# Kernel tuning notes

Measured on AMD Instinct MI355X. Metric: run time of the kernel, lower is better.

## Reference

```python
import jax, jax.numpy as jnp
import numpy as np
import math

N_HEADS = 8
TANH_CLIP = 10.0
TEMP = 1.0


def setup_inputs() -> dict:
    key = jax.random.key(0)
    ks = jax.random.split(key, 8)
    B, N, D = 256, 2048, 128
    node_embeddings = jax.random.normal(ks[0], (B, N, D), dtype=jnp.float32)
    W_node = jax.random.normal(ks[1], (D, 3 * D), dtype=jnp.float32) / math.sqrt(D)
    W_fixed = jax.random.normal(ks[2], (D, D), dtype=jnp.float32) / math.sqrt(D)
    W_step = jax.random.normal(ks[3], (2 * D, D), dtype=jnp.float32) / math.sqrt(2 * D)
    W_out = jax.random.normal(ks[4], (D, D), dtype=jnp.float32) / math.sqrt(D)
    first_idx = jax.random.randint(ks[5], (B,), 0, N, dtype=jnp.int32)
    last_idx = jax.random.randint(ks[6], (B,), 0, N, dtype=jnp.int32)
    mask = jax.random.bernoulli(ks[7], 0.5, (B, N))
    mask = mask.at[:, 0].set(False)  # guarantee at least one feasible node per row
    return {"node_embeddings": node_embeddings, "W_node": W_node, "W_fixed": W_fixed,
            "W_step": W_step, "W_out": W_out, "first_idx": first_idx,
            "last_idx": last_idx, "mask": mask}


def reference(node_embeddings, W_node, W_fixed, W_step, W_out, first_idx, last_idx, mask):
    B, N, D = node_embeddings.shape
    H = N_HEADS
    hd = D // H  # key_dim = val_dim = embed_dim / n_heads
    neg_inf = -jnp.inf

    # --- _precompute ---
    graph_embed = node_embeddings.mean(axis=1)                # [B, D]
    fixed_context = graph_embed @ W_fixed                     # [B, D]
    proj = node_embeddings @ W_node                           # [B, N, 3D]
    gK, gV, logit_K = jnp.split(proj, 3, axis=-1)             # each [B, N, D]
    gK = gK.reshape(B, N, H, hd).transpose(2, 0, 1, 3)        # [H, B, N, hd]
    gV = gV.reshape(B, N, H, hd).transpose(2, 0, 1, 3)        # [H, B, N, hd]

    # --- step context: cat(first node emb, last node emb) ---
    first_emb = jnp.take_along_axis(node_embeddings, first_idx[:, None, None].astype(jnp.int32), axis=1)[:, 0]  # [B, D]
    last_emb = jnp.take_along_axis(node_embeddings, last_idx[:, None, None].astype(jnp.int32), axis=1)[:, 0]
    step_ctx = jnp.concatenate([first_emb, last_emb], axis=-1)  # [B, 2D]
    query = fixed_context + step_ctx @ W_step                 # [B, D]

    # --- glimpse multi-head attention (n_query = 1, masked inner) ---
    Q = query.reshape(B, H, hd).transpose(1, 0, 2)            # [H, B, hd]
    compat = jnp.einsum('hbd,hbnd->hbn', Q, gK) / math.sqrt(hd)  # [H, B, N]
    compat = jnp.where(mask[None, :, :], neg_inf, compat)     # mask_inner=True
    attn = jax.nn.softmax(compat, axis=-1)
    heads = jnp.einsum('hbn,hbnd->hbd', attn, gV)             # [H, B, hd]
    glimpse = heads.transpose(1, 0, 2).reshape(B, D) @ W_out  # project_out, [B, D]

    # --- logits with tanh clipping and masking ---
    logits = jnp.einsum('bd,bnd->bn', glimpse, logit_K) / math.sqrt(D)  # [B, N]
    logits = jnp.tanh(logits) * TANH_CLIP
    logits = jnp.where(mask, neg_inf, logits)                 # mask_logits=True
    log_p = jax.nn.log_softmax(logits / TEMP, axis=-1)        # [B, N]
    return log_p
```

## Files before the change

kernel.cpp:

```cpp
#include <hip/hip_runtime.h>
#include <math.h>

#define B_ 256
#define N_ 2048
#define D_ 128

#define NEG_HUGE (-1.0e30f)

#define WSA_STRIDE 1040
#define WSA_SIZE (B_ * 8 * WSA_STRIDE)
#define WSB_OFF WSA_SIZE
#define WSB_SIZE (B_ * 8 * 2)
#define WSC_OFF (WSB_OFF + WSB_SIZE)

typedef __attribute__((ext_vector_type(8))) short bf16x8;
typedef __attribute__((ext_vector_type(4))) float f32x4;
typedef __attribute__((ext_vector_type(4))) unsigned short u16x4;
typedef __attribute__((ext_vector_type(2))) int i32x2;

__device__ __forceinline__ float wave_max64(float v) {
#pragma unroll
  for (int off = 32; off > 0; off >>= 1) v = fmaxf(v, __shfl_xor(v, off, 64));
  return v;
}
__device__ __forceinline__ float wave_sum64(float v) {
#pragma unroll
  for (int off = 32; off > 0; off >>= 1) v += __shfl_xor(v, off, 64);
  return v;
}
__device__ __forceinline__ unsigned short bf16rne(float f) {
  unsigned u = __float_as_uint(f);
  u += 0x7FFFu + ((u >> 16) & 1u);
  return (unsigned short)(u >> 16);
}

__global__ void __launch_bounds__(256) k_prep(const float* __restrict__ emb,
                                              float* __restrict__ buf) {
  const int b = blockIdx.x, s = blockIdx.y, t = threadIdx.x;
  const int f4 = t & 31, g = t >> 5;
  const size_t rowbase = (size_t)b * N_;
  float4 acc = make_float4(0.f, 0.f, 0.f, 0.f);
  int n = s * 256 + g;
#pragma unroll 8
  for (int i = 0; i < 32; ++i, n += 8) {
    const float4 v = *(const float4*)(emb + (rowbase + n) * D_ + f4 * 4);
    acc.x += v.x; acc.y += v.y; acc.z += v.z; acc.w += v.w;
  }
  __shared__ float4 red[256];
  red[t] = acc;
  __syncthreads();
  if (g == 0) {
    float4 r = red[f4];
#pragma unroll
    for (int j = 1; j < 8; ++j) {
      const float4 a = red[j * 32 + f4];
      r.x += a.x; r.y += a.y; r.z += a.z; r.w += a.w;
    }
    *(float4*)(buf + (size_t)b * N_ + s * 128 + f4 * 4) = r;
  }
}

__global__ void __launch_bounds__(384) k_query(const float* __restrict__ emb,
                                               const float* __restrict__ Wfix,
                                               const float* __restrict__ Wstep,
                                               const float* __restrict__ Wnode,
                                               const int* __restrict__ fidx,
                                               const int* __restrict__ lidx,
                                               float* __restrict__ buf) {
  const int b = blockIdx.x, t = threadIdx.x;
  __shared__ float x[384];
  __shared__ float part[3][128];
  __shared__ float q[128];

  if (t < 128) {
    float ssum = 0.f;
#pragma unroll
    for (int i = 0; i < 8; ++i) ssum += buf[(size_t)b * N_ + i * 128 + t];
    x[t] = ssum * (1.0f / 2048.0f);
  } else if (t < 256) {
    x[t] = emb[((size_t)b * N_ + fidx[b]) * D_ + (t - 128)];
  } else {
    x[t] = emb[((size_t)b * N_ + lidx[b]) * D_ + (t - 256)];
  }
  __syncthreads();

  {
    const int seg = t >> 7, j = t & 127;
    const float* xs = &x[seg * 128];
    const float* Wp = (seg == 0) ? (Wfix + j) : (Wstep + (seg == 1 ? 0 : 128 * 128) + j);
    float acc = 0.f;
#pragma unroll 8
    for (int k = 0; k < 128; ++k) acc = fmaf(xs[k], Wp[(size_t)k * 128], acc);
    part[seg][j] = acc;
  }
  __syncthreads();
  if (t < 128) q[t] = part[0][t] + part[1][t] + part[2][t];
  __syncthreads();

  if (t < 128) {
    const float* wrow = Wnode + (size_t)t * 384;
#pragma unroll
    for (int h = 0; h < 8; ++h) {
      float a = 0.f;
#pragma unroll
      for (int k = 0; k < 16; ++k) a = fmaf(q[h * 16 + k], wrow[h * 16 + k], a);
      buf[(size_t)b * N_ + 1024 + h * 128 + t] = a * 0.25f;
    }
  }
}

__global__ void __launch_bounds__(256) k_attn_m(const float* __restrict__ emb,
                                                const unsigned char* __restrict__ mask,
                                                const float* __restrict__ buf,
                                                float* __restrict__ wsA) {
  const int b = B_ - 1 - (int)blockIdx.x, s = 7 - (int)blockIdx.y;
  const int t = threadIdx.x;
  const int lane = t & 63, w = t >> 6;
  const int lg = lane >> 4, lc = lane & 15;

  __shared__ __align__(16) unsigned short eR[9216];
  __shared__ __align__(16) unsigned short pT[16 * 72];
  __shared__ float red0[4][16];
  __shared__ float red1[4][16];
  __shared__ float resc_s[16];
  __shared__ unsigned char mask_s[64];

  bf16x8 bq[4];
#pragma unroll
  for (int ks = 0; ks < 4; ++ks)
#pragma unroll
    for (int j = 0; j < 8; ++j) bq[ks][j] = 0;
  if (lc < 8) {
    const float* qrow = buf + (size_t)b * N_ + 1024 + lc * 128;
#pragma unroll
    for (int ks = 0; ks < 4; ++ks)
#pragma unroll
      for (int j = 0; j < 8; ++j)
        bq[ks][j] = (short)bf16rne(qrow[32 * ks + 8 * lg + j]);
  }

  float m_run = -INFINITY, l_run = 0.f;
  f32x4 wacc0 = {0.f, 0.f, 0.f, 0.f}, wacc1 = {0.f, 0.f, 0.f, 0.f};
  const float* embb = emb + ((size_t)b * N_ + s * 256) * D_;
  const unsigned char* mrow = mask + (size_t)b * N_ + s * 256;

  for (int tile = 0; tile < 4; ++tile) {
    {
      const float* src = embb + (size_t)tile * 64 * D_;
#pragma unroll
      for (int i = 0; i < 4; ++i) {
        const int gid = t + 256 * i;
        const int n = gid >> 4, d0 = (gid & 15) * 8;
        const float4 v0 = *(const float4*)(src + (size_t)n * D_ + d0);
        const float4 v1 = *(const float4*)(src + (size_t)n * D_ + d0 + 4);
        bf16x8 ev;
        ev[0] = (short)bf16rne(v0.x); ev[1] = (short)bf16rne(v0.y);
        ev[2] = (short)bf16rne(v0.z); ev[3] = (short)bf16rne(v0.w);
        ev[4] = (short)bf16rne(v1.x); ev[5] = (short)bf16rne(v1.y);
        ev[6] = (short)bf16rne(v1.z); ev[7] = (short)bf16rne(v1.w);
        const int widx = ((n >> 2) * 8 + (d0 >> 4)) * 72 + ((n & 3) << 4) + (d0 & 15);
        *(bf16x8*)&eR[widx] = ev;
      }
      if (t < 64) mask_s[t] = mrow[tile * 64 + t];
    }
    __syncthreads();

    f32x4 sAcc = {0.f, 0.f, 0.f, 0.f};
#pragma unroll
    for (int ks = 0; ks < 4; ++ks) {
      const int aidx = ((4 * w + (lc >> 2)) * 8 + 2 * ks + (lg >> 1)) * 72 +
                       ((lc & 3) << 4) + ((lg & 1) << 3);
      const bf16x8 af = *(const bf16x8*)&eR[aidx];
      sAcc = __builtin_amdgcn_mfma_f32_16x16x32_bf16(af, bq[ks], sAcc, 0, 0, 0);
    }

    float sv[4];
    bool mk[4];
    float tmax = -INFINITY;
#pragma unroll
    for (int r = 0; r < 4; ++r) {
      mk[r] = mask_s[16 * w + 4 * lg + r] != 0;
      sv[r] = mk[r] ? -INFINITY : sAcc[r];
      tmax = fmaxf(tmax, sv[r]);
    }
    tmax = fmaxf(tmax, __shfl_xor(tmax, 16, 64));
    tmax = fmaxf(tmax, __shfl_xor(tmax, 32, 64));
    if (lane < 16) red0[w][lc] = tmax;
    __syncthreads();

    const float m_tile = fmaxf(fmaxf(red0[0][lc], red0[1][lc]),
                               fmaxf(red0[2][lc], red0[3][lc]));
    const float m_new = fmaxf(m_run, m_tile);
    const float rsc = (m_new == -INFINITY) ? 1.f : __expf(m_run - m_new);
    float psum = 0.f;
    unsigned short pu[4];
#pragma unroll
    for (int r = 0; r < 4; ++r) {
      const float p = mk[r] ? 0.f : __expf(sv[r] - m_new);
      psum += p;
      pu[r] = bf16rne(p);
    }
    m_run = m_new;
    psum += __shfl_xor(psum, 16, 64);
    psum += __shfl_xor(psum, 32, 64);
    if (lane < 16) red1[w][lc] = psum;
    *(u16x4*)&pT[lc * 72 + 16 * w + 4 * lg] = (u16x4){pu[0], pu[1], pu[2], pu[3]};
    if (t < 16) resc_s[t] = rsc;
    __syncthreads();

    l_run = l_run * rsc + (red1[0][lc] + red1[1][lc] + red1[2][lc] + red1[3][lc]);

    {
      const float r0f = resc_s[4 * lg + 0], r1f = resc_s[4 * lg + 1];
      const float r2f = resc_s[4 * lg + 2], r3f = resc_s[4 * lg + 3];
      wacc0[0] *= r0f; wacc0[1] *= r1f; wacc0[2] *= r2f; wacc0[3] *= r3f;
      wacc1[0] *= r0f; wacc1[1] *= r1f; wacc1[2] *= r2f; wacc1[3] *= r3f;
    }

    i32x2 tb0a, tb0b, tb1a, tb1b, tb2a, tb2b, tb3a, tb3b;
    {
      const unsigned base00 = (unsigned)(unsigned long long)
          &eR[((0 + 2 * lg) * 8 + w) * 72 + lc];
      const unsigned base01 = (unsigned)(unsigned long long)
          &eR[((0 + 2 * lg) * 8 + (w + 4)) * 72 + lc];
      const unsigned base10 = (unsigned)(unsigned long long)
          &eR[((8 + 2 * lg) * 8 + w) * 72 + lc];
      const unsigned base11 = (unsigned)(unsigned long long)
          &eR[((8 + 2 * lg) * 8 + (w + 4)) * 72 + lc];
      asm volatile("ds_read_b64_tr_b16 %0, %2 offset:0\n\t"
                   "ds_read_b64_tr_b16 %1, %2 offset:1152"
                   : "=v"(tb0a), "=v"(tb0b) : "v"(base00));
      asm volatile("ds_read_b64_tr_b16 %0, %2 offset:0\n\t"
                   "ds_read_b64_tr_b16 %1, %2 offset:1152"
                   : "=v"(tb1a), "=v"(tb1b) : "v"(base01));
      asm volatile("ds_read_b64_tr_b16 %0, %2 offset:0\n\t"
                   "ds_read_b64_tr_b16 %1, %2 offset:1152"
                   : "=v"(tb2a), "=v"(tb2b) : "v"(base10));
      asm volatile("ds_read_b64_tr_b16 %0, %2 offset:0\n\t"
                   "ds_read_b64_tr_b16 %1, %2 offset:1152"
                   : "=v"(tb3a), "=v"(tb3b) : "v"(base11));
      asm volatile("s_waitcnt lgkmcnt(0)" ::: "memory");
      __builtin_amdgcn_sched_barrier(0);
    }
    {
      const bf16x8 pa0 = *(const bf16x8*)&pT[lc * 72 + 8 * lg];
      const bf16x8 pa1 = *(const bf16x8*)&pT[lc * 72 + 32 + 8 * lg];
      union { i32x2 d[2]; bf16x8 v; } u;
      u.d[0] = tb0a; u.d[1] = tb0b;
      wacc0 = __builtin_amdgcn_mfma_f32_16x16x32_bf16(pa0, u.v, wacc0, 0, 0, 0);
      u.d[0] = tb1a; u.d[1] = tb1b;
      wacc1 = __builtin_amdgcn_mfma_f32_16x16x32_bf16(pa0, u.v, wacc1, 0, 0, 0);
      u.d[0] = tb2a; u.d[1] = tb2b;
      wacc0 = __builtin_amdgcn_mfma_f32_16x16x32_bf16(pa1, u.v, wacc0, 0, 0, 0);
      u.d[0] = tb3a; u.d[1] = tb3b;
      wacc1 = __builtin_amdgcn_mfma_f32_16x16x32_bf16(pa1, u.v, wacc1, 0, 0, 0);
    }
    __syncthreads();
  }

  float* dst = wsA + (size_t)(b * 8 + s) * WSA_STRIDE;
  if (lg < 2) {
#pragma unroll
    for (int r = 0; r < 4; ++r) {
      const int h = 4 * lg + r;
      dst[16 + h * 128 + 16 * w + lc] = wacc0[r];
      dst[16 + h * 128 + 16 * (w + 4) + lc] = wacc1[r];
    }
  }
  if (t < 8) { dst[t] = m_run; dst[8 + t] = l_run; }
}

__global__ void __launch_bounds__(256) k_attn_comb(const float* __restrict__ Wnode,
                                                   const float* __restrict__ Wout,
                                                   const float* __restrict__ wsA,
                                                   float* __restrict__ wsC) {
  const int b = blockIdx.x, t = threadIdx.x;
  const int j = t & 127, hh = t >> 7;
  const float* base = wsA + (size_t)b * 8 * WSA_STRIDE;
  __shared__ float Ls[8], scale[8][8];
  __shared__ float wl[8 * 128], heads[128], glim[128];
  __shared__ float part2[2][128];

  if (t < 8) {
    float M = -INFINITY;
#pragma unroll
    for (int s = 0; s < 8; ++s) M = fmaxf(M, base[s * WSA_STRIDE + t]);
    float L = 0.f;
#pragma unroll
    for (int s = 0; s < 8; ++s) {
      const float m = base[s * WSA_STRIDE + t];
      const float sc = (m == -INFINITY) ? 0.f : __expf(m - M);
      scale[s][t] = sc;
      L = fmaf(base[s * WSA_STRIDE + 8 + t], sc, L);
    }
    Ls[t] = L;
  }
  __syncthreads();

#pragma unroll
  for (int k = 0; k < 4; ++k) {
    const int idx = t + 256 * k;
    const int h = idx >> 7, d = idx & 127;
    float acc = 0.f;
#pragma unroll
    for (int s = 0; s < 8; ++s)
      acc = fmaf(scale[s][h], base[s * WSA_STRIDE + 16 + h * 128 + d], acc);
    wl[idx] = acc;
  }
  __syncthreads();

  {
    const int h = j >> 4, kk = j & 15;
    const float* wp = Wnode + 128 + h * 16 + kk;
    float acc = 0.f;
#pragma unroll 8
    for (int d = 64 * hh; d < 64 * hh + 64; ++d)
      acc = fmaf(wl[h * 128 + d], wp[(size_t)d * 384], acc);
    part2[hh][j] = acc;
  }
  __syncthreads();
  if (t < 128) heads[t] = (part2[0][t] + part2[1][t]) / Ls[t >> 4];
  __syncthreads();

  {
    float acc = 0.f;
#pragma unroll 8
    for (int k = 64 * hh; k < 64 * hh + 64; ++k)
      acc = fmaf(heads[k], Wout[(size_t)k * 128 + j], acc);
    part2[hh][j] = acc;
  }
  __syncthreads();
  if (t < 128) glim[t] = part2[0][t] + part2[1][t];
  __syncthreads();

  {
    const float* wr = Wnode + (size_t)j * 384 + 256;
    float acc = 0.f;
#pragma unroll 8
    for (int k = 64 * hh; k < 64 * hh + 64; ++k)
      acc = fmaf(wr[k], glim[k], acc);
    part2[hh][j] = acc;
  }
  __syncthreads();
  if (t < 128)
    wsC[(size_t)b * 128 + t] = (part2[0][t] + part2[1][t]) * 0.08838834764831845f;
}

__global__ void __launch_bounds__(256) k_logits_part(const float* __restrict__ emb,
                                                     const unsigned char* __restrict__ mask,
                                                     const float* __restrict__ wsC,
                                                     float* __restrict__ buf,
                                                     float* __restrict__ wsB) {
  const int b = blockIdx.x, s = blockIdx.y;
  const int t = threadIdx.x, lane = t & 63, w = t >> 6;
  __shared__ float lg[64];
  const float4 cf = ((const float4*)(wsC + (size_t)b * 128))[t & 31];
  const float* embb = emb + ((size_t)b * N_ + s * 256) * D_;
  const unsigned char* mrow = mask + (size_t)b * N_ + s * 256;
  float mr = NEG_HUGE, sr = 0.f;

  for (int tile = 0; tile < 4; ++tile) {
    const int n0 = tile * 64;
#pragma unroll
    for (int i = 0; i < 8; ++i) {
      const int gid = t + 256 * i;
      const int r = gid >> 5, c = (gid & 31) * 4;
      const float4 e = *(const float4*)(embb + (size_t)(n0 + r) * D_ + c);
      float p = fmaf(e.x, cf.x, fmaf(e.y, cf.y, fmaf(e.z, cf.z, e.w * cf.w)));
      p += __shfl_xor(p, 16, 64);
      p += __shfl_xor(p, 8, 64);
      p += __shfl_xor(p, 4, 64);
      p += __shfl_xor(p, 2, 64);
      p += __shfl_xor(p, 1, 64);
      if ((t & 31) == 0) lg[r] = p;
    }
    __syncthreads();

    const bool mk = mrow[n0 + lane] != 0;
    const float x = lg[lane];
    const float ex = __expf(2.f * x);
    const float val = mk ? NEG_HUGE : (10.f - __fdividef(20.f, ex + 1.f));
    const float tm = wave_max64(val);
    const float mn = fmaxf(mr, tm);
    sr = sr * __expf(mr - mn) + wave_sum64(mk ? 0.f : __expf(val - mn));
    mr = mn;
    if (w == 0) buf[(size_t)b * N_ + s * 256 + n0 + lane] = val;
    __syncthreads();
  }
  if (t == 0) {
    wsB[(size_t)(b * 8 + s) * 2] = mr;
    wsB[(size_t)(b * 8 + s) * 2 + 1] = sr;
  }
}

__global__ void __launch_bounds__(256) k_norm(const float* __restrict__ wsB,
                                              float* __restrict__ buf) {
  const int b = blockIdx.x, s = blockIdx.y, t = threadIdx.x;
  float M = NEG_HUGE;
#pragma unroll
  for (int q = 0; q < 8; ++q) M = fmaxf(M, wsB[(size_t)(b * 8 + q) * 2]);
  float S = 0.f;
#pragma unroll
  for (int q = 0; q < 8; ++q) {
    const float m = wsB[(size_t)(b * 8 + q) * 2];
    S += wsB[(size_t)(b * 8 + q) * 2 + 1] * __expf(m - M);
  }
  const float LS = M + logf(S);
  const size_t idx = (size_t)b * N_ + s * 256 + t;
  const float v = buf[idx];
  buf[idx] = (v <= -1.0e29f) ? NEG_HUGE : (v - LS);
}

extern "C" void kernel_launch(void* const* d_in, const int* in_sizes, int n_in,
                              void* d_out, int out_size, void* d_ws, size_t ws_size,
                              hipStream_t stream) {
  (void)in_sizes; (void)n_in; (void)out_size; (void)ws_size;
  const float* emb = (const float*)d_in[0];
  const float* Wnode = (const float*)d_in[1];
  const float* Wfix = (const float*)d_in[2];
  const float* Wstep = (const float*)d_in[3];
  const float* Wout = (const float*)d_in[4];
  const int* fidx = (const int*)d_in[5];
  const int* lidx = (const int*)d_in[6];
  const unsigned char* mask = (const unsigned char*)d_in[7];
  float* buf = (float*)d_out;
  float* ws = (float*)d_ws;

  k_prep<<<dim3(B_, 8), 256, 0, stream>>>(emb, buf);
  k_query<<<B_, 384, 0, stream>>>(emb, Wfix, Wstep, Wnode, fidx, lidx, buf);
  k_attn_m<<<dim3(B_, 8), 256, 0, stream>>>(emb, mask, buf, ws);
  k_attn_comb<<<B_, 256, 0, stream>>>(Wnode, Wout, ws, ws + WSC_OFF);
  k_logits_part<<<dim3(B_, 8), 256, 0, stream>>>(emb, mask, ws + WSC_OFF, buf, ws + WSB_OFF);
  k_norm<<<dim3(B_, 8), 256, 0, stream>>>(ws + WSB_OFF, buf);
}
```

Baseline: 161.1 us.

## Fuse all stages into persistent kernel with grid barriers and bf16 embedding copy

Replaces the six-kernel pipeline with one persistent kernel of 1024 blocks that runs the stages in sequence, separated by software grid barriers built on atomics. The first pass, which reads the fp32 embeddings to compute the mean, also writes a bf16 copy to workspace. The attention and logits passes then read that copy instead of re-reading the fp32 data, roughly halving their memory traffic. In exchange it adds a 128 MB workspace write, a deadlock risk if the 1024 blocks are not all resident at once, and reduced precision in the logits dot product.

```diff
diff --git a/kernel.cpp b/kernel.cpp
--- a/kernel.cpp
+++ b/kernel.cpp
@@ -4,14 +4,22 @@
 #define B_ 256
 #define N_ 2048
 #define D_ 128
+#define NSEG 2048
+#define GRID_MEGA 1024
 
 #define NEG_HUGE (-1.0e30f)
 
+#define WSE_BYTES ((size_t)B_ * N_ * D_ * 2)
+#define WSQ_OFF 262144
+#define WSA_OFF 524288
+#define WSB_OFF_M 2654208
+#define WSC_OFF_M 2658304
+#define BAR_OFF 2691072
+#define WS_NEED_BYTES (WSE_BYTES + (size_t)(BAR_OFF + 8) * 4)
+
 #define WSA_STRIDE 1040
-#define WSA_SIZE (B_ * 8 * WSA_STRIDE)
-#define WSB_OFF WSA_SIZE
-#define WSB_SIZE (B_ * 8 * 2)
-#define WSC_OFF (WSB_OFF + WSB_SIZE)
+#define FB_WSB_OFF (B_ * 8 * WSA_STRIDE)
+#define FB_WSC_OFF (FB_WSB_OFF + B_ * 8 * 2)
 
 typedef __attribute__((ext_vector_type(8))) short bf16x8;
 typedef __attribute__((ext_vector_type(4))) float f32x4;
@@ -32,6 +40,409 @@
   unsigned u = __float_as_uint(f);
   u += 0x7FFFu + ((u >> 16) & 1u);
   return (unsigned short)(u >> 16);
+}
+__device__ __forceinline__ float bflo(unsigned u) { return __uint_as_float(u << 16); }
+__device__ __forceinline__ float bfhi(unsigned u) { return __uint_as_float(u & 0xFFFF0000u); }
+
+__device__ __forceinline__ void grid_barrier(unsigned* bar, unsigned nb) {
+  __syncthreads();
+  if (threadIdx.x == 0) {
+    const unsigned mygen = atomicAdd(&bar[1], 0u);
+    __threadfence();
+    const unsigned arrived = atomicAdd(&bar[0], 1u) + 1u;
+    if (arrived == nb) {
+      atomicExch(&bar[0], 0u);
+      __threadfence();
+      atomicAdd(&bar[1], 1u);
+    } else {
+      while (atomicAdd(&bar[1], 0u) == mygen) { __builtin_amdgcn_s_sleep(8); }
+    }
+    __threadfence();
+  }
+  __syncthreads();
+}
+
+__global__ void __launch_bounds__(256, 4) k_mega(
+    const float* __restrict__ emb, const float* __restrict__ Wnode,
+    const float* __restrict__ Wfix, const float* __restrict__ Wstep,
+    const float* __restrict__ Wout, const int* __restrict__ fidx,
+    const int* __restrict__ lidx, const unsigned char* __restrict__ mask,
+    float* __restrict__ buf, unsigned short* __restrict__ wsE,
+    float* __restrict__ wsF, unsigned* __restrict__ bar) {
+  const int g = blockIdx.x, t = threadIdx.x;
+  const unsigned nb = gridDim.x;
+  float* wsM = wsF;
+  float* wsQ = wsF + WSQ_OFF;
+  float* wsA = wsF + WSA_OFF;
+  float* wsB = wsF + WSB_OFF_M;
+  float* wsC = wsF + WSC_OFF_M;
+
+  __shared__ __align__(16) unsigned char smem[21504];
+
+  for (int seg = g; seg < NSEG; seg += nb) {
+    const int b = seg >> 3, s = seg & 7;
+    const int f4 = t & 31, gg = t >> 5;
+    const size_t rowbase = (size_t)b * N_;
+    float4 acc = make_float4(0.f, 0.f, 0.f, 0.f);
+    int n = s * 256 + gg;
+#pragma unroll 8
+    for (int i = 0; i < 32; ++i, n += 8) {
+      const float4 v = *(const float4*)(emb + (rowbase + n) * D_ + f4 * 4);
+      acc.x += v.x; acc.y += v.y; acc.z += v.z; acc.w += v.w;
+      ushort4 o;
+      o.x = bf16rne(v.x); o.y = bf16rne(v.y); o.z = bf16rne(v.z); o.w = bf16rne(v.w);
+      *(ushort4*)(wsE + (rowbase + n) * D_ + f4 * 4) = o;
+    }
+    float4* red = (float4*)smem;
+    __syncthreads();
+    red[t] = acc;
+    __syncthreads();
+    if (gg == 0) {
+      float4 r = red[f4];
+#pragma unroll
+      for (int j = 1; j < 8; ++j) {
+        const float4 a = red[j * 32 + f4];
+        r.x += a.x; r.y += a.y; r.z += a.z; r.w += a.w;
+      }
+      *(float4*)(wsM + (size_t)(b * 8 + s) * 128 + f4 * 4) = r;
+    }
+  }
+  grid_barrier(bar, nb);
+
+  for (int b = g; b < B_; b += nb) {
+    float* ge = (float*)smem;
+    float* fe = ge + 128;
+    float* le = ge + 256;
+    float* pq = ge + 384;
+    float* q = ge + 640;
+    if (t < 128) {
+      float ssum = 0.f;
+#pragma unroll
+      for (int i = 0; i < 8; ++i) ssum += wsM[(size_t)(b * 8 + i) * 128 + t];
+      ge[t] = ssum * (1.0f / 2048.0f);
+      fe[t] = emb[((size_t)b * N_ + fidx[b]) * D_ + t];
+      le[t] = emb[((size_t)b * N_ + lidx[b]) * D_ + t];
+    }
+    __syncthreads();
+    {
+      const int j = t & 127, h2 = t >> 7;
+      float acc = 0.f;
+#pragma unroll 4
+      for (int k = 64 * h2; k < 64 * h2 + 64; ++k) {
+        acc = fmaf(ge[k], Wfix[k * 128 + j], acc);
+        acc = fmaf(fe[k], Wstep[k * 128 + j], acc);
+        acc = fmaf(le[k], Wstep[(128 + k) * 128 + j], acc);
+      }
+      pq[h2 * 128 + j] = acc;
+    }
+    __syncthreads();
+    if (t < 128) q[t] = pq[t] + pq[128 + t];
+    __syncthreads();
+    if (t < 128) {
+      const float* wrow = Wnode + (size_t)t * 384;
+#pragma unroll
+      for (int h = 0; h < 8; ++h) {
+        float a = 0.f;
+#pragma unroll
+        for (int k = 0; k < 16; ++k) a = fmaf(q[h * 16 + k], wrow[h * 16 + k], a);
+        wsQ[(size_t)b * 1024 + h * 128 + t] = a * 0.25f;
+      }
+    }
+    __syncthreads();
+  }
+  grid_barrier(bar, nb);
+
+  {
+    unsigned short* eR = (unsigned short*)smem;
+    unsigned short* pT = (unsigned short*)(smem + 18432);
+    float* red0 = (float*)(smem + 20736);
+    float* red1 = (float*)(smem + 20992);
+    float* resc = (float*)(smem + 21248);
+    unsigned char* mask_s = smem + 21312;
+    const int lane = t & 63, w = t >> 6;
+    const int lg = lane >> 4, lc = lane & 15;
+
+    for (int seg = g; seg < NSEG; seg += nb) {
+      const int b = seg >> 3, s = seg & 7;
+      bf16x8 bq[4];
+#pragma unroll
+      for (int ks = 0; ks < 4; ++ks)
+#pragma unroll
+        for (int j = 0; j < 8; ++j) bq[ks][j] = 0;
+      if (lc < 8) {
+        const float* qrow = wsQ + (size_t)b * 1024 + lc * 128;
+#pragma unroll
+        for (int ks = 0; ks < 4; ++ks)
+#pragma unroll
+          for (int j = 0; j < 8; ++j)
+            bq[ks][j] = (short)bf16rne(qrow[32 * ks + 8 * lg + j]);
+      }
+
+      float m_run = -INFINITY, l_run = 0.f;
+      f32x4 wacc0 = {0.f, 0.f, 0.f, 0.f}, wacc1 = {0.f, 0.f, 0.f, 0.f};
+      const unsigned short* embB = wsE + ((size_t)b * N_ + s * 256) * D_;
+      const unsigned char* mrow = mask + (size_t)b * N_ + s * 256;
+
+      for (int tile = 0; tile < 4; ++tile) {
+        __syncthreads();
+#pragma unroll
+        for (int i = 0; i < 4; ++i) {
+          const int gid = t + 256 * i;
+          const int n = gid >> 4, d0 = (gid & 15) * 8;
+          const int widx =
+              ((n >> 2) * 8 + (d0 >> 4)) * 72 + ((n & 3) << 4) + (d0 & 15);
+          const uint4 u =
+              *(const uint4*)(embB + ((size_t)tile * 64 + n) * D_ + d0);
+          *(uint4*)&eR[widx] = u;
+        }
+        if (t < 64) mask_s[t] = mrow[tile * 64 + t];
+        __syncthreads();
+
+        f32x4 sAcc = {0.f, 0.f, 0.f, 0.f};
+#pragma unroll
+        for (int ks = 0; ks < 4; ++ks) {
+          const int aidx = ((4 * w + (lc >> 2)) * 8 + 2 * ks + (lg >> 1)) * 72 +
+                           ((lc & 3) << 4) + ((lg & 1) << 3);
+          const bf16x8 af = *(const bf16x8*)&eR[aidx];
+          sAcc = __builtin_amdgcn_mfma_f32_16x16x32_bf16(af, bq[ks], sAcc, 0, 0, 0);
+        }
+
+        float sv[4];
+        bool mk[4];
+        float tmax = -INFINITY;
+#pragma unroll
+        for (int r = 0; r < 4; ++r) {
+          mk[r] = mask_s[16 * w + 4 * lg + r] != 0;
+          sv[r] = mk[r] ? -INFINITY : sAcc[r];
+          tmax = fmaxf(tmax, sv[r]);
+        }
+        tmax = fmaxf(tmax, __shfl_xor(tmax, 16, 64));
+        tmax = fmaxf(tmax, __shfl_xor(tmax, 32, 64));
+        if (lane < 16) red0[w * 16 + lc] = tmax;
+        __syncthreads();
+
+        const float m_tile = fmaxf(fmaxf(red0[lc], red0[16 + lc]),
+                                   fmaxf(red0[32 + lc], red0[48 + lc]));
+        const float m_new = fmaxf(m_run, m_tile);
+        const float rsc = (m_new == -INFINITY) ? 1.f : __expf(m_run - m_new);
+        float psum = 0.f;
+        unsigned short pu[4];
+#pragma unroll
+        for (int r = 0; r < 4; ++r) {
+          const float p = mk[r] ? 0.f : __expf(sv[r] - m_new);
+          psum += p;
+          pu[r] = bf16rne(p);
+        }
+        m_run = m_new;
+        psum += __shfl_xor(psum, 16, 64);
+        psum += __shfl_xor(psum, 32, 64);
+        if (lane < 16) red1[w * 16 + lc] = psum;
+        *(u16x4*)&pT[lc * 72 + 16 * w + 4 * lg] = (u16x4){pu[0], pu[1], pu[2], pu[3]};
+        if (t < 16) resc[t] = rsc;
+        __syncthreads();
+
+        l_run = l_run * rsc +
+                (red1[lc] + red1[16 + lc] + red1[32 + lc] + red1[48 + lc]);
+        {
+          const float r0f = resc[4 * lg + 0], r1f = resc[4 * lg + 1];
+          const float r2f = resc[4 * lg + 2], r3f = resc[4 * lg + 3];
+          wacc0[0] *= r0f; wacc0[1] *= r1f; wacc0[2] *= r2f; wacc0[3] *= r3f;
+          wacc1[0] *= r0f; wacc1[1] *= r1f; wacc1[2] *= r2f; wacc1[3] *= r3f;
+        }
+
+        i32x2 tb0a, tb0b, tb1a, tb1b, tb2a, tb2b, tb3a, tb3b;
+        {
+          const unsigned base00 = (unsigned)(unsigned long long)
+              &eR[((0 + 2 * lg) * 8 + w) * 72 + lc];
+          const unsigned base01 = (unsigned)(unsigned long long)
+              &eR[((0 + 2 * lg) * 8 + (w + 4)) * 72 + lc];
+          const unsigned base10 = (unsigned)(unsigned long long)
+              &eR[((8 + 2 * lg) * 8 + w) * 72 + lc];
+          const unsigned base11 = (unsigned)(unsigned long long)
+              &eR[((8 + 2 * lg) * 8 + (w + 4)) * 72 + lc];
+          asm volatile("ds_read_b64_tr_b16 %0, %2 offset:0\n\t"
+                       "ds_read_b64_tr_b16 %1, %2 offset:1152"
+                       : "=v"(tb0a), "=v"(tb0b) : "v"(base00));
+          asm volatile("ds_read_b64_tr_b16 %0, %2 offset:0\n\t"
+                       "ds_read_b64_tr_b16 %1, %2 offset:1152"
+                       : "=v"(tb1a), "=v"(tb1b) : "v"(base01));
+          asm volatile("ds_read_b64_tr_b16 %0, %2 offset:0\n\t"
+                       "ds_read_b64_tr_b16 %1, %2 offset:1152"
+                       : "=v"(tb2a), "=v"(tb2b) : "v"(base10));
+          asm volatile("ds_read_b64_tr_b16 %0, %2 offset:0\n\t"
+                       "ds_read_b64_tr_b16 %1, %2 offset:1152"
+                       : "=v"(tb3a), "=v"(tb3b) : "v"(base11));
+          asm volatile("s_waitcnt lgkmcnt(0)" ::: "memory");
+          __builtin_amdgcn_sched_barrier(0);
+        }
+        {
+          const bf16x8 pa0 = *(const bf16x8*)&pT[lc * 72 + 8 * lg];
+          const bf16x8 pa1 = *(const bf16x8*)&pT[lc * 72 + 32 + 8 * lg];
+          union { i32x2 d[2]; bf16x8 v; } u;
+          u.d[0] = tb0a; u.d[1] = tb0b;
+          wacc0 = __builtin_amdgcn_mfma_f32_16x16x32_bf16(pa0, u.v, wacc0, 0, 0, 0);
+          u.d[0] = tb1a; u.d[1] = tb1b;
+          wacc1 = __builtin_amdgcn_mfma_f32_16x16x32_bf16(pa0, u.v, wacc1, 0, 0, 0);
+          u.d[0] = tb2a; u.d[1] = tb2b;
+          wacc0 = __builtin_amdgcn_mfma_f32_16x16x32_bf16(pa1, u.v, wacc0, 0, 0, 0);
+          u.d[0] = tb3a; u.d[1] = tb3b;
+          wacc1 = __builtin_amdgcn_mfma_f32_16x16x32_bf16(pa1, u.v, wacc1, 0, 0, 0);
+        }
+        __syncthreads();
+      }
+
+      float* dst = wsA + (size_t)(b * 8 + s) * WSA_STRIDE;
+      if (lg < 2) {
+#pragma unroll
+        for (int r = 0; r < 4; ++r) {
+          const int h = 4 * lg + r;
+          dst[16 + h * 128 + 16 * w + lc] = wacc0[r];
+          dst[16 + h * 128 + 16 * (w + 4) + lc] = wacc1[r];
+        }
+      }
+      if (t < 8) { dst[t] = m_run; dst[8 + t] = l_run; }
+      __syncthreads();
+    }
+  }
+  grid_barrier(bar, nb);
+
+  for (int b = g; b < B_; b += nb) {
+    float* Ls = (float*)smem;
+    float* scale = Ls + 8;
+    float* wl = scale + 64;
+    float* heads = wl + 1024;
+    float* glim = heads + 128;
+    float* p2 = glim + 128;
+    const int j = t & 127, hh = t >> 7;
+    const float* base = wsA + (size_t)b * 8 * WSA_STRIDE;
+
+    if (t < 8) {
+      float M = -INFINITY;
+#pragma unroll
+      for (int s = 0; s < 8; ++s) M = fmaxf(M, base[s * WSA_STRIDE + t]);
+      float L = 0.f;
+#pragma unroll
+      for (int s = 0; s < 8; ++s) {
+        const float m = base[s * WSA_STRIDE + t];
+        const float sc = (m == -INFINITY) ? 0.f : __expf(m - M);
+        scale[s * 8 + t] = sc;
+        L = fmaf(base[s * WSA_STRIDE + 8 + t], sc, L);
+      }
+      Ls[t] = L;
+    }
+    __syncthreads();
+#pragma unroll
+    for (int k = 0; k < 4; ++k) {
+      const int idx = t + 256 * k;
+      const int h = idx >> 7, d = idx & 127;
+      float acc = 0.f;
+#pragma unroll
+      for (int s = 0; s < 8; ++s)
+        acc = fmaf(scale[s * 8 + h], base[s * WSA_STRIDE + 16 + h * 128 + d], acc);
+      wl[idx] = acc;
+    }
+    __syncthreads();
+    {
+      const int h = j >> 4, kk = j & 15;
+      const float* wp = Wnode + 128 + h * 16 + kk;
+      float acc = 0.f;
+#pragma unroll 8
+      for (int d = 64 * hh; d < 64 * hh + 64; ++d)
+        acc = fmaf(wl[h * 128 + d], wp[(size_t)d * 384], acc);
+      p2[hh * 128 + j] = acc;
+    }
+    __syncthreads();
+    if (t < 128) heads[t] = (p2[t] + p2[128 + t]) / Ls[t >> 4];
+    __syncthreads();
+    {
+      float acc = 0.f;
+#pragma unroll 8
+      for (int k = 64 * hh; k < 64 * hh + 64; ++k)
+        acc = fmaf(heads[k], Wout[(size_t)k * 128 + j], acc);
+      p2[hh * 128 + j] = acc;
+    }
+    __syncthreads();
+    if (t < 128) glim[t] = p2[t] + p2[128 + t];
+    __syncthreads();
+    {
+      const float* wr = Wnode + (size_t)j * 384 + 256;
+      float acc = 0.f;
+#pragma unroll 8
+      for (int k = 64 * hh; k < 64 * hh + 64; ++k) acc = fmaf(wr[k], glim[k], acc);
+      p2[hh * 128 + j] = acc;
+    }
+    __syncthreads();
+    if (t < 128)
+      wsC[(size_t)b * 128 + t] = (p2[t] + p2[128 + t]) * 0.08838834764831845f;
+    __syncthreads();
+  }
+  grid_barrier(bar, nb);
+
+  {
+    float* lgs = (float*)smem;
+    const int lane = t & 63, w4 = t >> 6;
+    for (int seg = g; seg < NSEG; seg += nb) {
+      const int b = seg >> 3, s = seg & 7;
+      const float4* c4 = (const float4*)(wsC + (size_t)b * 128);
+      const float4 cfa = c4[(t & 15) * 2];
+      const float4 cfb = c4[(t & 15) * 2 + 1];
+      const unsigned short* embB = wsE + ((size_t)b * N_ + s * 256) * D_;
+      const unsigned char* mrow = mask + (size_t)b * N_ + s * 256;
+      float mr = NEG_HUGE, sr = 0.f;
+      for (int tile = 0; tile < 4; ++tile) {
+        const int n0 = tile * 64;
+#pragma unroll
+        for (int i = 0; i < 4; ++i) {
+          const int gid = t + 256 * i;
+          const int r = gid >> 4, c8 = (gid & 15) * 8;
+          const uint4 u = *(const uint4*)(embB + (size_t)(n0 + r) * D_ + c8);
+          float p = bflo(u.x) * cfa.x + bfhi(u.x) * cfa.y;
+          p = fmaf(bflo(u.y), cfa.z, p); p = fmaf(bfhi(u.y), cfa.w, p);
+          p = fmaf(bflo(u.z), cfb.x, p); p = fmaf(bfhi(u.z), cfb.y, p);
+          p = fmaf(bflo(u.w), cfb.z, p); p = fmaf(bfhi(u.w), cfb.w, p);
+          p += __shfl_xor(p, 8, 64);
+          p += __shfl_xor(p, 4, 64);
+          p += __shfl_xor(p, 2, 64);
+          p += __shfl_xor(p, 1, 64);
+          if ((t & 15) == 0) lgs[r] = p;
+        }
+        __syncthreads();
+        const bool mk = mrow[n0 + lane] != 0;
+        const float x = lgs[lane];
+        const float ex = __expf(2.f * x);
+        const float val = mk ? NEG_HUGE : (10.f - __fdividef(20.f, ex + 1.f));
+        const float tm = wave_max64(val);
+        const float mn = fmaxf(mr, tm);
+        sr = sr * __expf(mr - mn) + wave_sum64(mk ? 0.f : __expf(val - mn));
+        mr = mn;
+        if (w4 == 0) buf[(size_t)b * N_ + s * 256 + n0 + lane] = val;
+        __syncthreads();
+      }
+      if (t == 0) {
+        wsB[(size_t)(b * 8 + s) * 2] = mr;
+        wsB[(size_t)(b * 8 + s) * 2 + 1] = sr;
+      }
+      __syncthreads();
+    }
+  }
+  grid_barrier(bar, nb);
+
+  for (int seg = g; seg < NSEG; seg += nb) {
+    const int b = seg >> 3, s = seg & 7;
+    float M = NEG_HUGE;
+#pragma unroll
+    for (int qq = 0; qq < 8; ++qq) M = fmaxf(M, wsB[(size_t)(b * 8 + qq) * 2]);
+    float S = 0.f;
+#pragma unroll
+    for (int qq = 0; qq < 8; ++qq) {
+      const float m = wsB[(size_t)(b * 8 + qq) * 2];
+      S += wsB[(size_t)(b * 8 + qq) * 2 + 1] * __expf(m - M);
+    }
+    const float LS = M + logf(S);
+    const size_t idx = (size_t)b * N_ + s * 256 + t;
+    const float v = buf[idx];
+    buf[idx] = (v <= -1.0e29f) ? NEG_HUGE : (v - LS);
+  }
 }
 
 __global__ void __launch_bounds__(256) k_prep(const float* __restrict__ emb,
@@ -71,7 +482,6 @@
   __shared__ float x[384];
   __shared__ float part[3][128];
   __shared__ float q[128];
-
   if (t < 128) {
     float ssum = 0.f;
 #pragma unroll
@@ -83,7 +493,6 @@
     x[t] = emb[((size_t)b * N_ + lidx[b]) * D_ + (t - 256)];
   }
   __syncthreads();
-
   {
     const int seg = t >> 7, j = t & 127;
     const float* xs = &x[seg * 128];
@@ -96,7 +505,6 @@
   __syncthreads();
   if (t < 128) q[t] = part[0][t] + part[1][t] + part[2][t];
   __syncthreads();
-
   if (t < 128) {
     const float* wrow = Wnode + (size_t)t * 384;
 #pragma unroll
@@ -113,18 +521,16 @@
                                                 const unsigned char* __restrict__ mask,
                                                 const float* __restrict__ buf,
                                                 float* __restrict__ wsA) {
-  const int b = B_ - 1 - (int)blockIdx.x, s = 7 - (int)blockIdx.y;
+  const int b = blockIdx.x, s = blockIdx.y;
   const int t = threadIdx.x;
   const int lane = t & 63, w = t >> 6;
   const int lg = lane >> 4, lc = lane & 15;
-
   __shared__ __align__(16) unsigned short eR[9216];
   __shared__ __align__(16) unsigned short pT[16 * 72];
   __shared__ float red0[4][16];
   __shared__ float red1[4][16];
   __shared__ float resc_s[16];
   __shared__ unsigned char mask_s[64];
-
   bf16x8 bq[4];
 #pragma unroll
   for (int ks = 0; ks < 4; ++ks)
@@ -138,12 +544,10 @@
       for (int j = 0; j < 8; ++j)
         bq[ks][j] = (short)bf16rne(qrow[32 * ks + 8 * lg + j]);
   }
-
   float m_run = -INFINITY, l_run = 0.f;
   f32x4 wacc0 = {0.f, 0.f, 0.f, 0.f}, wacc1 = {0.f, 0.f, 0.f, 0.f};
   const float* embb = emb + ((size_t)b * N_ + s * 256) * D_;
   const unsigned char* mrow = mask + (size_t)b * N_ + s * 256;
-
   for (int tile = 0; tile < 4; ++tile) {
     {
       const float* src = embb + (size_t)tile * 64 * D_;
@@ -164,7 +568,6 @@
       if (t < 64) mask_s[t] = mrow[tile * 64 + t];
     }
     __syncthreads();
-
     f32x4 sAcc = {0.f, 0.f, 0.f, 0.f};
 #pragma unroll
     for (int ks = 0; ks < 4; ++ks) {
@@ -173,7 +576,6 @@
       const bf16x8 af = *(const bf16x8*)&eR[aidx];
       sAcc = __builtin_amdgcn_mfma_f32_16x16x32_bf16(af, bq[ks], sAcc, 0, 0, 0);
     }
-
     float sv[4];
     bool mk[4];
     float tmax = -INFINITY;
@@ -187,7 +589,6 @@
     tmax = fmaxf(tmax, __shfl_xor(tmax, 32, 64));
     if (lane < 16) red0[w][lc] = tmax;
     __syncthreads();
-
     const float m_tile = fmaxf(fmaxf(red0[0][lc], red0[1][lc]),
                                fmaxf(red0[2][lc], red0[3][lc]));
     const float m_new = fmaxf(m_run, m_tile);
@@ -207,16 +608,13 @@
     *(u16x4*)&pT[lc * 72 + 16 * w + 4 * lg] = (u16x4){pu[0], pu[1], pu[2], pu[3]};
     if (t < 16) resc_s[t] = rsc;
     __syncthreads();
-
     l_run = l_run * rsc + (red1[0][lc] + red1[1][lc] + red1[2][lc] + red1[3][lc]);
-
     {
       const float r0f = resc_s[4 * lg + 0], r1f = resc_s[4 * lg + 1];
       const float r2f = resc_s[4 * lg + 2], r3f = resc_s[4 * lg + 3];
       wacc0[0] *= r0f; wacc0[1] *= r1f; wacc0[2] *= r2f; wacc0[3] *= r3f;
       wacc1[0] *= r0f; wacc1[1] *= r1f; wacc1[2] *= r2f; wacc1[3] *= r3f;
     }
-
     i32x2 tb0a, tb0b, tb1a, tb1b, tb2a, tb2b, tb3a, tb3b;
     {
       const unsigned base00 = (unsigned)(unsigned long long)
@@ -257,7 +655,6 @@
     }
     __syncthreads();
   }
-
   float* dst = wsA + (size_t)(b * 8 + s) * WSA_STRIDE;
   if (lg < 2) {
 #pragma unroll
@@ -280,7 +677,6 @@
   __shared__ float Ls[8], scale[8][8];
   __shared__ float wl[8 * 128], heads[128], glim[128];
   __shared__ float part2[2][128];
-
   if (t < 8) {
     float M = -INFINITY;
 #pragma unroll
@@ -296,7 +692,6 @@
     Ls[t] = L;
   }
   __syncthreads();
-
 #pragma unroll
   for (int k = 0; k < 4; ++k) {
     const int idx = t + 256 * k;
@@ -308,7 +703,6 @@
     wl[idx] = acc;
   }
   __syncthreads();
-
   {
     const int h = j >> 4, kk = j & 15;
     const float* wp = Wnode + 128 + h * 16 + kk;
@@ -321,7 +715,6 @@
   __syncthreads();
   if (t < 128) heads[t] = (part2[0][t] + part2[1][t]) / Ls[t >> 4];
   __syncthreads();
-
   {
     float acc = 0.f;
 #pragma unroll 8
@@ -332,13 +725,11 @@
   __syncthreads();
   if (t < 128) glim[t] = part2[0][t] + part2[1][t];
   __syncthreads();
-
   {
     const float* wr = Wnode + (size_t)j * 384 + 256;
     float acc = 0.f;
 #pragma unroll 8
-    for (int k = 64 * hh; k < 64 * hh + 64; ++k)
-      acc = fmaf(wr[k], glim[k], acc);
+    for (int k = 64 * hh; k < 64 * hh + 64; ++k) acc = fmaf(wr[k], glim[k], acc);
     part2[hh][j] = acc;
   }
   __syncthreads();
@@ -358,7 +749,6 @@
   const float* embb = emb + ((size_t)b * N_ + s * 256) * D_;
   const unsigned char* mrow = mask + (size_t)b * N_ + s * 256;
   float mr = NEG_HUGE, sr = 0.f;
-
   for (int tile = 0; tile < 4; ++tile) {
     const int n0 = tile * 64;
 #pragma unroll
@@ -375,7 +765,6 @@
       if ((t & 31) == 0) lg[r] = p;
     }
     __syncthreads();
-
     const bool mk = mrow[n0 + lane] != 0;
     const float x = lg[lane];
     const float ex = __expf(2.f * x);
@@ -414,7 +803,7 @@
 extern "C" void kernel_launch(void* const* d_in, const int* in_sizes, int n_in,
                               void* d_out, int out_size, void* d_ws, size_t ws_size,
                               hipStream_t stream) {
-  (void)in_sizes; (void)n_in; (void)out_size; (void)ws_size;
+  (void)in_sizes; (void)n_in; (void)out_size;
   const float* emb = (const float*)d_in[0];
   const float* Wnode = (const float*)d_in[1];
   const float* Wfix = (const float*)d_in[2];
@@ -424,12 +813,25 @@
   const int* lidx = (const int*)d_in[6];
   const unsigned char* mask = (const unsigned char*)d_in[7];
   float* buf = (float*)d_out;
-  float* ws = (float*)d_ws;
-
-  k_prep<<<dim3(B_, 8), 256, 0, stream>>>(emb, buf);
-  k_query<<<B_, 384, 0, stream>>>(emb, Wfix, Wstep, Wnode, fidx, lidx, buf);
-  k_attn_m<<<dim3(B_, 8), 256, 0, stream>>>(emb, mask, buf, ws);
-  k_attn_comb<<<B_, 256, 0, stream>>>(Wnode, Wout, ws, ws + WSC_OFF);
-  k_logits_part<<<dim3(B_, 8), 256, 0, stream>>>(emb, mask, ws + WSC_OFF, buf, ws + WSB_OFF);
-  k_norm<<<dim3(B_, 8), 256, 0, stream>>>(ws + WSB_OFF, buf);
-}
+
+  int occ = 0;
+  (void)hipOccupancyMaxActiveBlocksPerMultiprocessor(&occ, k_mega, 256, 0);
+
+  if (occ >= 4 && ws_size >= WS_NEED_BYTES) {
+    unsigned short* wsE = (unsigned short*)d_ws;
+    float* wsF = (float*)((char*)d_ws + WSE_BYTES);
+    unsigned* bar = (unsigned*)(wsF + BAR_OFF);
+    hipMemsetAsync(bar, 0, 8, stream);
+    k_mega<<<GRID_MEGA, 256, 0, stream>>>(emb, Wnode, Wfix, Wstep, Wout, fidx,
+                                          lidx, mask, buf, wsE, wsF, bar);
+  } else {
+    float* ws = (float*)d_ws;
+    k_prep<<<dim3(B_, 8), 256, 0, stream>>>(emb, buf);
+    k_query<<<B_, 384, 0, stream>>>(emb, Wfix, Wstep, Wnode, fidx, lidx, buf);
+    k_attn_m<<<dim3(B_, 8), 256, 0, stream>>>(emb, mask, buf, ws);
+    k_attn_comb<<<B_, 256, 0, stream>>>(Wnode, Wout, ws, ws + FB_WSC_OFF);
+    k_logits_part<<<dim3(B_, 8), 256, 0, stream>>>(emb, mask, ws + FB_WSC_OFF, buf,
+                                                   ws + FB_WSB_OFF);
+    k_norm<<<dim3(B_, 8), 256, 0, stream>>>(ws + FB_WSB_OFF, buf);
+  }
+}
```

Result: no change. 160.2 us (-0.6%).

## Fuse combine and normalize stages into last-arriving blocks via atomic counters

Applied to the files above, without the earlier changes.

Removes the separate k_attn_comb and k_norm launches. Each block increments a per-batch atomic counter, and the last of the 8 split blocks performs the cross-split combine (attention merge plus projections) or the final log-softmax normalization. This saves two kernel launches and their tail/ramp gaps. The cost is a memset for the counters and serialized tail work in one block per batch. The block index order reversal in k_attn_m is also dropped.

```diff
diff --git a/kernel.cpp b/kernel.cpp
--- a/kernel.cpp
+++ b/kernel.cpp
@@ -8,10 +8,10 @@
 #define NEG_HUGE (-1.0e30f)
 
 #define WSA_STRIDE 1040
-#define WSA_SIZE (B_ * 8 * WSA_STRIDE)
-#define WSB_OFF WSA_SIZE
-#define WSB_SIZE (B_ * 8 * 2)
-#define WSC_OFF (WSB_OFF + WSB_SIZE)
+#define WSB_OFF (B_ * 8 * WSA_STRIDE)
+#define WSC_OFF (WSB_OFF + B_ * 8 * 2)
+#define FLAGS_OFF (WSC_OFF + B_ * D_)
+#define WS_NEED_BYTES ((size_t)(FLAGS_OFF + 512) * 4)
 
 typedef __attribute__((ext_vector_type(8))) short bf16x8;
 typedef __attribute__((ext_vector_type(4))) float f32x4;
@@ -71,7 +71,6 @@
   __shared__ float x[384];
   __shared__ float part[3][128];
   __shared__ float q[128];
-
   if (t < 128) {
     float ssum = 0.f;
 #pragma unroll
@@ -83,7 +82,6 @@
     x[t] = emb[((size_t)b * N_ + lidx[b]) * D_ + (t - 256)];
   }
   __syncthreads();
-
   {
     const int seg = t >> 7, j = t & 127;
     const float* xs = &x[seg * 128];
@@ -96,7 +94,6 @@
   __syncthreads();
   if (t < 128) q[t] = part[0][t] + part[1][t] + part[2][t];
   __syncthreads();
-
   if (t < 128) {
     const float* wrow = Wnode + (size_t)t * 384;
 #pragma unroll
@@ -112,18 +109,22 @@
 __global__ void __launch_bounds__(256) k_attn_m(const float* __restrict__ emb,
                                                 const unsigned char* __restrict__ mask,
                                                 const float* __restrict__ buf,
-                                                float* __restrict__ wsA) {
-  const int b = B_ - 1 - (int)blockIdx.x, s = 7 - (int)blockIdx.y;
+                                                const float* __restrict__ Wnode,
+                                                const float* __restrict__ Wout,
+                                                float* __restrict__ wsA,
+                                                float* __restrict__ wsC,
+                                                unsigned* __restrict__ cprog) {
+  const int b = blockIdx.x, s = blockIdx.y;
   const int t = threadIdx.x;
   const int lane = t & 63, w = t >> 6;
   const int lg = lane >> 4, lc = lane & 15;
-
   __shared__ __align__(16) unsigned short eR[9216];
   __shared__ __align__(16) unsigned short pT[16 * 72];
-  __shared__ float red0[4][16];
-  __shared__ float red1[4][16];
-  __shared__ float resc_s[16];
+  __shared__ float red0[64];
+  __shared__ float red1[64];
+  __shared__ float resc[16];
   __shared__ unsigned char mask_s[64];
+  __shared__ unsigned sh_old;
 
   bf16x8 bq[4];
 #pragma unroll
@@ -138,12 +139,10 @@
       for (int j = 0; j < 8; ++j)
         bq[ks][j] = (short)bf16rne(qrow[32 * ks + 8 * lg + j]);
   }
-
   float m_run = -INFINITY, l_run = 0.f;
   f32x4 wacc0 = {0.f, 0.f, 0.f, 0.f}, wacc1 = {0.f, 0.f, 0.f, 0.f};
   const float* embb = emb + ((size_t)b * N_ + s * 256) * D_;
   const unsigned char* mrow = mask + (size_t)b * N_ + s * 256;
-
   for (int tile = 0; tile < 4; ++tile) {
     {
       const float* src = embb + (size_t)tile * 64 * D_;
@@ -164,7 +163,6 @@
       if (t < 64) mask_s[t] = mrow[tile * 64 + t];
     }
     __syncthreads();
-
     f32x4 sAcc = {0.f, 0.f, 0.f, 0.f};
 #pragma unroll
     for (int ks = 0; ks < 4; ++ks) {
@@ -173,7 +171,6 @@
       const bf16x8 af = *(const bf16x8*)&eR[aidx];
       sAcc = __builtin_amdgcn_mfma_f32_16x16x32_bf16(af, bq[ks], sAcc, 0, 0, 0);
     }
-
     float sv[4];
     bool mk[4];
     float tmax = -INFINITY;
@@ -185,11 +182,10 @@
     }
     tmax = fmaxf(tmax, __shfl_xor(tmax, 16, 64));
     tmax = fmaxf(tmax, __shfl_xor(tmax, 32, 64));
-    if (lane < 16) red0[w][lc] = tmax;
-    __syncthreads();
-
-    const float m_tile = fmaxf(fmaxf(red0[0][lc], red0[1][lc]),
-                               fmaxf(red0[2][lc], red0[3][lc]));
+    if (lane < 16) red0[w * 16 + lc] = tmax;
+    __syncthreads();
+    const float m_tile = fmaxf(fmaxf(red0[lc], red0[16 + lc]),
+                               fmaxf(red0[32 + lc], red0[48 + lc]));
     const float m_new = fmaxf(m_run, m_tile);
     const float rsc = (m_new == -INFINITY) ? 1.f : __expf(m_run - m_new);
     float psum = 0.f;
@@ -203,20 +199,17 @@
     m_run = m_new;
     psum += __shfl_xor(psum, 16, 64);
     psum += __shfl_xor(psum, 32, 64);
-    if (lane < 16) red1[w][lc] = psum;
+    if (lane < 16) red1[w * 16 + lc] = psum;
     *(u16x4*)&pT[lc * 72 + 16 * w + 4 * lg] = (u16x4){pu[0], pu[1], pu[2], pu[3]};
-    if (t < 16) resc_s[t] = rsc;
-    __syncthreads();
-
-    l_run = l_run * rsc + (red1[0][lc] + red1[1][lc] + red1[2][lc] + red1[3][lc]);
-
-    {
-      const float r0f = resc_s[4 * lg + 0], r1f = resc_s[4 * lg + 1];
-      const float r2f = resc_s[4 * lg + 2], r3f = resc_s[4 * lg + 3];
+    if (t < 16) resc[t] = rsc;
+    __syncthreads();
+    l_run = l_run * rsc + (red1[lc] + red1[16 + lc] + red1[32 + lc] + red1[48 + lc]);
+    {
+      const float r0f = resc[4 * lg + 0], r1f = resc[4 * lg + 1];
+      const float r2f = resc[4 * lg + 2], r3f = resc[4 * lg + 3];
       wacc0[0] *= r0f; wacc0[1] *= r1f; wacc0[2] *= r2f; wacc0[3] *= r3f;
       wacc1[0] *= r0f; wacc1[1] *= r1f; wacc1[2] *= r2f; wacc1[3] *= r3f;
     }
-
     i32x2 tb0a, tb0b, tb1a, tb1b, tb2a, tb2b, tb3a, tb3b;
     {
       const unsigned base00 = (unsigned)(unsigned long long)
@@ -257,7 +250,6 @@
     }
     __syncthreads();
   }
-
   float* dst = wsA + (size_t)(b * 8 + s) * WSA_STRIDE;
   if (lg < 2) {
 #pragma unroll
@@ -268,97 +260,95 @@
     }
   }
   if (t < 8) { dst[t] = m_run; dst[8 + t] = l_run; }
-}
-
-__global__ void __launch_bounds__(256) k_attn_comb(const float* __restrict__ Wnode,
-                                                   const float* __restrict__ Wout,
-                                                   const float* __restrict__ wsA,
-                                                   float* __restrict__ wsC) {
-  const int b = blockIdx.x, t = threadIdx.x;
-  const int j = t & 127, hh = t >> 7;
-  const float* base = wsA + (size_t)b * 8 * WSA_STRIDE;
-  __shared__ float Ls[8], scale[8][8];
-  __shared__ float wl[8 * 128], heads[128], glim[128];
-  __shared__ float part2[2][128];
-
-  if (t < 8) {
-    float M = -INFINITY;
-#pragma unroll
-    for (int s = 0; s < 8; ++s) M = fmaxf(M, base[s * WSA_STRIDE + t]);
-    float L = 0.f;
-#pragma unroll
-    for (int s = 0; s < 8; ++s) {
-      const float m = base[s * WSA_STRIDE + t];
-      const float sc = (m == -INFINITY) ? 0.f : __expf(m - M);
-      scale[s][t] = sc;
-      L = fmaf(base[s * WSA_STRIDE + 8 + t], sc, L);
-    }
-    Ls[t] = L;
-  }
-  __syncthreads();
-
-#pragma unroll
-  for (int k = 0; k < 4; ++k) {
-    const int idx = t + 256 * k;
-    const int h = idx >> 7, d = idx & 127;
-    float acc = 0.f;
-#pragma unroll
-    for (int s = 0; s < 8; ++s)
-      acc = fmaf(scale[s][h], base[s * WSA_STRIDE + 16 + h * 128 + d], acc);
-    wl[idx] = acc;
-  }
-  __syncthreads();
-
-  {
-    const int h = j >> 4, kk = j & 15;
-    const float* wp = Wnode + 128 + h * 16 + kk;
-    float acc = 0.f;
+  __syncthreads();
+  if (t == 0) { __threadfence(); sh_old = atomicAdd(&cprog[b], 1u); }
+  __syncthreads();
+
+  if (sh_old == 7u) {
+    __threadfence();
+    float* Ls = red0;
+    float* scale = red1;
+    float* wl = (float*)eR;
+    float* heads = wl + 1024;
+    float* glim = heads + 128;
+    float* p2 = glim + 128;
+    const int j = t & 127, hh = t >> 7;
+    const float* base = wsA + (size_t)b * 8 * WSA_STRIDE;
+    if (t < 8) {
+      float M = -INFINITY;
+#pragma unroll
+      for (int q = 0; q < 8; ++q) M = fmaxf(M, base[q * WSA_STRIDE + t]);
+      float L = 0.f;
+#pragma unroll
+      for (int q = 0; q < 8; ++q) {
+        const float m = base[q * WSA_STRIDE + t];
+        const float sc = (m == -INFINITY) ? 0.f : __expf(m - M);
+        scale[q * 8 + t] = sc;
+        L = fmaf(base[q * WSA_STRIDE + 8 + t], sc, L);
+      }
+      Ls[t] = L;
+    }
+    __syncthreads();
+#pragma unroll
+    for (int k = 0; k < 4; ++k) {
+      const int idx = t + 256 * k;
+      const int h = idx >> 7, d = idx & 127;
+      float acc = 0.f;
+#pragma unroll
+      for (int q = 0; q < 8; ++q)
+        acc = fmaf(scale[q * 8 + h], base[q * WSA_STRIDE + 16 + h * 128 + d], acc);
+      wl[idx] = acc;
+    }
+    __syncthreads();
+    {
+      const int h = j >> 4, kk = j & 15;
+      const float* wp = Wnode + 128 + h * 16 + kk;
+      float acc = 0.f;
 #pragma unroll 8
-    for (int d = 64 * hh; d < 64 * hh + 64; ++d)
-      acc = fmaf(wl[h * 128 + d], wp[(size_t)d * 384], acc);
-    part2[hh][j] = acc;
-  }
-  __syncthreads();
-  if (t < 128) heads[t] = (part2[0][t] + part2[1][t]) / Ls[t >> 4];
-  __syncthreads();
-
-  {
-    float acc = 0.f;
+      for (int d = 64 * hh; d < 64 * hh + 64; ++d)
+        acc = fmaf(wl[h * 128 + d], wp[(size_t)d * 384], acc);
+      p2[hh * 128 + j] = acc;
+    }
+    __syncthreads();
+    if (t < 128) heads[t] = (p2[t] + p2[128 + t]) / Ls[t >> 4];
+    __syncthreads();
+    {
+      float acc = 0.f;
 #pragma unroll 8
-    for (int k = 64 * hh; k < 64 * hh + 64; ++k)
-      acc = fmaf(heads[k], Wout[(size_t)k * 128 + j], acc);
-    part2[hh][j] = acc;
-  }
-  __syncthreads();
-  if (t < 128) glim[t] = part2[0][t] + part2[1][t];
-  __syncthreads();
-
-  {
-    const float* wr = Wnode + (size_t)j * 384 + 256;
-    float acc = 0.f;
+      for (int k = 64 * hh; k < 64 * hh + 64; ++k)
+        acc = fmaf(heads[k], Wout[(size_t)k * 128 + j], acc);
+      p2[hh * 128 + j] = acc;
+    }
+    __syncthreads();
+    if (t < 128) glim[t] = p2[t] + p2[128 + t];
+    __syncthreads();
+    {
+      const float* wr = Wnode + (size_t)j * 384 + 256;
+      float acc = 0.f;
 #pragma unroll 8
-    for (int k = 64 * hh; k < 64 * hh + 64; ++k)
-      acc = fmaf(wr[k], glim[k], acc);
-    part2[hh][j] = acc;
-  }
-  __syncthreads();
-  if (t < 128)
-    wsC[(size_t)b * 128 + t] = (part2[0][t] + part2[1][t]) * 0.08838834764831845f;
+      for (int k = 64 * hh; k < 64 * hh + 64; ++k) acc = fmaf(wr[k], glim[k], acc);
+      p2[hh * 128 + j] = acc;
+    }
+    __syncthreads();
+    if (t < 128)
+      wsC[(size_t)b * 128 + t] = (p2[t] + p2[128 + t]) * 0.08838834764831845f;
+  }
 }
 
 __global__ void __launch_bounds__(256) k_logits_part(const float* __restrict__ emb,
                                                      const unsigned char* __restrict__ mask,
                                                      const float* __restrict__ wsC,
                                                      float* __restrict__ buf,
-                                                     float* __restrict__ wsB) {
+                                                     float* __restrict__ wsB,
+                                                     unsigned* __restrict__ eprog) {
   const int b = blockIdx.x, s = blockIdx.y;
   const int t = threadIdx.x, lane = t & 63, w = t >> 6;
   __shared__ float lg[64];
+  __shared__ unsigned sh_old;
   const float4 cf = ((const float4*)(wsC + (size_t)b * 128))[t & 31];
   const float* embb = emb + ((size_t)b * N_ + s * 256) * D_;
   const unsigned char* mrow = mask + (size_t)b * N_ + s * 256;
   float mr = NEG_HUGE, sr = 0.f;
-
   for (int tile = 0; tile < 4; ++tile) {
     const int n0 = tile * 64;
 #pragma unroll
@@ -375,7 +365,6 @@
       if ((t & 31) == 0) lg[r] = p;
     }
     __syncthreads();
-
     const bool mk = mrow[n0 + lane] != 0;
     const float x = lg[lane];
     const float ex = __expf(2.f * x);
@@ -391,24 +380,29 @@
     wsB[(size_t)(b * 8 + s) * 2] = mr;
     wsB[(size_t)(b * 8 + s) * 2 + 1] = sr;
   }
-}
-
-__global__ void __launch_bounds__(256) k_norm(const float* __restrict__ wsB,
-                                              float* __restrict__ buf) {
-  const int b = blockIdx.x, s = blockIdx.y, t = threadIdx.x;
-  float M = NEG_HUGE;
-#pragma unroll
-  for (int q = 0; q < 8; ++q) M = fmaxf(M, wsB[(size_t)(b * 8 + q) * 2]);
-  float S = 0.f;
-#pragma unroll
-  for (int q = 0; q < 8; ++q) {
-    const float m = wsB[(size_t)(b * 8 + q) * 2];
-    S += wsB[(size_t)(b * 8 + q) * 2 + 1] * __expf(m - M);
-  }
-  const float LS = M + logf(S);
-  const size_t idx = (size_t)b * N_ + s * 256 + t;
-  const float v = buf[idx];
-  buf[idx] = (v <= -1.0e29f) ? NEG_HUGE : (v - LS);
+  __syncthreads();
+  if (t == 0) { __threadfence(); sh_old = atomicAdd(&eprog[b], 1u); }
+  __syncthreads();
+
+  if (sh_old == 7u) {
+    __threadfence();
+    float M = NEG_HUGE;
+#pragma unroll
+    for (int q = 0; q < 8; ++q) M = fmaxf(M, wsB[(size_t)(b * 8 + q) * 2]);
+    float S = 0.f;
+#pragma unroll
+    for (int q = 0; q < 8; ++q) {
+      const float m = wsB[(size_t)(b * 8 + q) * 2];
+      S += wsB[(size_t)(b * 8 + q) * 2 + 1] * __expf(m - M);
+    }
+    const float LS = M + logf(S);
+#pragma unroll
+    for (int i = 0; i < 8; ++i) {
+      const size_t idx = (size_t)b * N_ + i * 256 + t;
+      const float v = buf[idx];
+      buf[idx] = (v <= -1.0e29f) ? NEG_HUGE : (v - LS);
+    }
+  }
 }
 
 extern "C" void kernel_launch(void* const* d_in, const int* in_sizes, int n_in,
@@ -425,11 +419,13 @@
   const unsigned char* mask = (const unsigned char*)d_in[7];
   float* buf = (float*)d_out;
   float* ws = (float*)d_ws;
-
+  unsigned* flg = (unsigned*)(ws + FLAGS_OFF);
+
+  hipMemsetAsync(flg, 0, 512 * 4, stream);
   k_prep<<<dim3(B_, 8), 256, 0, stream>>>(emb, buf);
   k_query<<<B_, 384, 0, stream>>>(emb, Wfix, Wstep, Wnode, fidx, lidx, buf);
-  k_attn_m<<<dim3(B_, 8), 256, 0, stream>>>(emb, mask, buf, ws);
-  k_attn_comb<<<B_, 256, 0, stream>>>(Wnode, Wout, ws, ws + WSC_OFF);
-  k_logits_part<<<dim3(B_, 8), 256, 0, stream>>>(emb, mask, ws + WSC_OFF, buf, ws + WSB_OFF);
-  k_norm<<<dim3(B_, 8), 256, 0, stream>>>(ws + WSB_OFF, buf);
-}
+  k_attn_m<<<dim3(B_, 8), 256, 0, stream>>>(emb, mask, buf, Wnode, Wout, ws,
+                                            ws + WSC_OFF, flg);
+  k_logits_part<<<dim3(B_, 8), 256, 0, stream>>>(emb, mask, ws + WSC_OFF, buf,
+                                                 ws + WSB_OFF, flg + 256);
+}
```

Measured after the change: 358.0 us. 2.22x slower.
